# Kernel tuning notes

Measured on AMD Instinct MI355X. Metric: run time of the kernel, lower is better.

The kernel has to match this reference:

```python
import jax, jax.numpy as jnp
import numpy as np

D_MODEL = 1024
N_HEAD = 16
D_K = D_MODEL // N_HEAD
B, S = 2, 2048


def setup_inputs() -> dict:
    key = jax.random.key(0)
    ks = jax.random.split(key, 12)
    sc = 1.0 / np.sqrt(D_MODEL)
    return {
        "q": jax.random.normal(ks[0], (B, S, D_MODEL), jnp.float32),
        "k": jax.random.normal(ks[1], (B, S, D_MODEL), jnp.float32),
        "v": jax.random.normal(ks[2], (B, S, D_MODEL), jnp.float32),
        "mask": jax.random.randint(ks[3], (B, S, S), 0, 2, jnp.int32),
        # learned params (torch Linear convention: y = x @ W + b with W pre-transposed)
        "wq": jax.random.normal(ks[4], (D_MODEL, D_MODEL), jnp.float32) * sc,
        "bq": jax.random.normal(ks[5], (D_MODEL,), jnp.float32) * sc,
        "wk": jax.random.normal(ks[6], (D_MODEL, D_MODEL), jnp.float32) * sc,  # no bias
        "wv": jax.random.normal(ks[7], (D_MODEL, D_MODEL), jnp.float32) * sc,
        "bv": jax.random.normal(ks[8], (D_MODEL,), jnp.float32) * sc,
        "wf": jax.random.normal(ks[9], (D_MODEL, D_MODEL), jnp.float32) * sc,
        "bf": jax.random.normal(ks[10], (D_MODEL,), jnp.float32) * sc,
    }


def reference(q, k, v, mask, wq, bq, wk, wv, bv, wf, bf):
    bs = q.shape[0]
    temperature = jnp.asarray(D_K ** 0.5, q.dtype)
    # projections -> [b, h, s, d_k]
    qh = (q @ wq + bq).reshape(bs, -1, N_HEAD, D_K).transpose(0, 2, 1, 3)
    kh = (k @ wk).reshape(bs, -1, N_HEAD, D_K).transpose(0, 2, 1, 3)
    vh = (v @ wv + bv).reshape(bs, -1, N_HEAD, D_K).transpose(0, 2, 1, 3)
    # scores [b, h, sq, sk]
    attn = jnp.einsum("bhqd,bhkd->bhqk", qh, kh) / temperature
    m0 = (mask[:, None, :, :] == 0)  # mask==0 -> masked out, broadcast over heads
    attn = jnp.where(m0, -jnp.inf, attn)
    attn = jax.nn.softmax(attn, axis=-1)
    attn = jnp.where(m0, 0.0, attn)
    out = jnp.einsum("bhqk,bhkd->bhqd", attn, vh)
    out = out.transpose(0, 2, 1, 3).reshape(bs, -1, D_MODEL)
    return out @ wf + bf  # dropout is identity in eval mode
```

## Files before the change

kernel.cpp:

```cpp
#include <hip/hip_runtime.h>

#define D_MODEL 1024
#define NHEAD   16
#define DK      64
#define BATCH   2
#define SEQ     2048

typedef __attribute__((ext_vector_type(8))) short bf16x8;
typedef __attribute__((ext_vector_type(4))) short bf16x4;
typedef __attribute__((ext_vector_type(4))) float f32x4;
typedef __attribute__((ext_vector_type(2))) int i32x2;

#define QSCALE 0.18033688011f

__device__ __forceinline__ unsigned short f2b(float x) {
  unsigned u = __builtin_bit_cast(unsigned, x);
  u = (u + 0x7fffu + ((u >> 16) & 1u)) >> 16;
  return (unsigned short)u;
}
__device__ __forceinline__ unsigned short f2b_rhu(float x) {
  return (unsigned short)((__builtin_bit_cast(unsigned, x) + 0x8000u) >> 16);
}
__device__ __forceinline__ int pk2(float a, float b) {
  unsigned ua = __builtin_bit_cast(unsigned, a) + 0x8000u;
  unsigned ub = __builtin_bit_cast(unsigned, b) + 0x8000u;
  return (int)__builtin_amdgcn_perm(ub, ua, 0x07060302u);
}
__device__ __forceinline__ int pk2u(unsigned ua, unsigned ub) {
  return (int)__builtin_amdgcn_perm(ub + 0x8000u, ua + 0x8000u, 0x07060302u);
}

typedef const __attribute__((address_space(1))) void* gas_p;
typedef __attribute__((address_space(3))) void* las_p;
__device__ __forceinline__ void gll16(const void* g, void* l) {
  __builtin_amdgcn_global_load_lds((gas_p)g, (las_p)l, 16, 0, 0);
}

__device__ __forceinline__ f32x4 mfma16(bf16x4 a, bf16x4 b, f32x4 c) {
#if __has_builtin(__builtin_amdgcn_mfma_f32_16x16x16bf16_1k)
  return __builtin_amdgcn_mfma_f32_16x16x16bf16_1k(a, b, c, 0, 0, 0);
#else
  f32x4 d;
  asm("v_mfma_f32_16x16x16_bf16 %0, %1, %2, %3" : "=v"(d) : "v"(a), "v"(b), "v"(c));
  return d;
#endif
}

__global__ __launch_bounds__(256) void prep_kernel(
    const float* __restrict__ q, const float* __restrict__ k, const float* __restrict__ v,
    unsigned short* __restrict__ qb, unsigned short* __restrict__ kb,
    unsigned short* __restrict__ vb,
    const float* __restrict__ wq, const float* __restrict__ wk,
    const float* __restrict__ wv, const float* __restrict__ wf,
    unsigned short* __restrict__ wqt, unsigned short* __restrict__ wkt,
    unsigned short* __restrict__ wvt, unsigned short* __restrict__ wft,
    const int* __restrict__ mask, unsigned long long* __restrict__ mbits) {
  int bid = blockIdx.x, t = threadIdx.x;
  if (bid < 6144) {
    int by = bid >> 11, bx = bid & 2047;
    const float* src = by == 0 ? q : (by == 1 ? k : v);
    unsigned short* dst = by == 0 ? qb : (by == 1 ? kb : vb);
    size_t i = ((size_t)bx * 256 + t) * 8;
    float4 x0 = *(const float4*)&src[i];
    float4 x1 = *(const float4*)&src[i + 4];
    int4 w;
    w.x = pk2(x0.x, x0.y); w.y = pk2(x0.z, x0.w);
    w.z = pk2(x1.x, x1.y); w.w = pk2(x1.z, x1.w);
    *(int4*)&dst[i] = w;
  } else if (bid < 7168) {
    __shared__ float tile[64][65];
    int idx = bid - 6144;
    int bz = idx >> 8, by = (idx >> 4) & 15, bx = idx & 15;
    const float* w; unsigned short* wt;
    switch (bz) {
      case 0: w = wq; wt = wqt; break;
      case 1: w = wk; wt = wkt; break;
      case 2: w = wv; wt = wvt; break;
      default: w = wf; wt = wft; break;
    }
    int r0 = by * 64, c0 = bx * 64;
    for (int i = 0; i < 16; ++i) {
      int idx2 = t + i * 256; int r = idx2 >> 6, c = idx2 & 63;
      tile[r][c] = w[(size_t)(r0 + r) * D_MODEL + c0 + c];
    }
    __syncthreads();
    for (int i = 0; i < 16; ++i) {
      int idx2 = t + i * 256; int r = idx2 >> 6, c = idx2 & 63;
      wt[(size_t)(c0 + r) * D_MODEL + r0 + c] = f2b(tile[c][r]);
    }
  } else {
    int idx = bid - 7168;
    int lane = t & 63, wave = t >> 6;
    size_t base = ((size_t)idx * 4 + wave) * 256;
    unsigned long long b0 = __ballot(mask[base + lane] != 0);
    unsigned long long b1 = __ballot(mask[base + 64 + lane] != 0);
    unsigned long long b2 = __ballot(mask[base + 128 + lane] != 0);
    unsigned long long b3 = __ballot(mask[base + 192 + lane] != 0);
    if (lane == 0) {
      unsigned long long* p = &mbits[(size_t)idx * 16 + wave * 4];
      p[0] = b0; p[1] = b1; p[2] = b2; p[3] = b3;
    }
  }
}

__global__ __launch_bounds__(256) void gemm_qkv_kernel(
    const unsigned short* __restrict__ qb, const unsigned short* __restrict__ kb,
    const unsigned short* __restrict__ vb,
    const unsigned short* __restrict__ wqt, const unsigned short* __restrict__ wkt,
    const unsigned short* __restrict__ wvt,
    const float* __restrict__ bq, const float* __restrict__ bv,
    unsigned short* __restrict__ qh, unsigned short* __restrict__ kh,
    unsigned short* __restrict__ vt) {
  __shared__ unsigned short SB[16640];
  int bid = blockIdx.x;
  int xcd = bid & 7, slot = bid >> 3;
  int mi = slot & 3, zn = slot >> 2;
  int z = zn >> 3;
  int n0 = (zn & 7) * 128;
  int m0 = (mi * 8 + xcd) * 128;
  const unsigned short* A; const unsigned short* Bt;
  switch (z) {
    case 0:  A = qb; Bt = wqt; break;
    case 1:  A = kb; Bt = wkt; break;
    default: A = vb; Bt = wvt; break;
  }
  int t = threadIdx.x, lane = t & 63, wave = t >> 6;
  int l16 = lane & 15, quad = lane >> 4;
  int wm = (wave & 1) * 64, wn = (wave >> 1) * 64;
  f32x4 zero = {0.f, 0.f, 0.f, 0.f};
  f32x4 acc[4][4];
  for (int mt = 0; mt < 4; ++mt) for (int nt = 0; nt < 4; ++nt) acc[mt][nt] = zero;

  int drow = lane >> 2, dcol = (lane & 3) * 8;
  const unsigned short* asrc = A  + (size_t)(m0 + wave * 32 + drow) * D_MODEL + dcol;
  const unsigned short* bsrc = Bt + (size_t)(n0 + wave * 32 + drow) * D_MODEL + dcol;
  int dst = wave * 1024 + lane * 8;

#pragma unroll
  for (int g = 0; g < 2; ++g) {
    gll16(asrc + (size_t)(g * 16) * D_MODEL, &SB[dst + g * 512]);
    gll16(bsrc + (size_t)(g * 16) * D_MODEL, &SB[4096 + dst + g * 512]);
  }
  for (int it = 0; it < 32; ++it) {
    __syncthreads();
    if (it + 1 < 32) {
      int nb = ((it + 1) & 1) * 8192, kn = (it + 1) * 32;
#pragma unroll
      for (int g = 0; g < 2; ++g) {
        gll16(asrc + (size_t)(g * 16) * D_MODEL + kn, &SB[nb + dst + g * 512]);
        gll16(bsrc + (size_t)(g * 16) * D_MODEL + kn, &SB[nb + 4096 + dst + g * 512]);
      }
    }
    int cb = (it & 1) * 8192;
    bf16x8 a[4], b[4];
    for (int mt = 0; mt < 4; ++mt)
      a[mt] = *(const bf16x8*)&SB[cb + (wm + mt * 16 + l16) * 32 + quad * 8];
    for (int nt = 0; nt < 4; ++nt)
      b[nt] = *(const bf16x8*)&SB[cb + 4096 + (wn + nt * 16 + l16) * 32 + quad * 8];
    for (int mt = 0; mt < 4; ++mt)
      for (int nt = 0; nt < 4; ++nt)
        acc[mt][nt] = __builtin_amdgcn_mfma_f32_16x16x32_bf16(a[mt], b[nt], acc[mt][nt], 0, 0, 0);
  }

  if (z == 2) {
    __syncthreads();
#pragma unroll
    for (int nt = 0; nt < 4; ++nt) {
      int col = wn + nt * 16 + l16;
      float bb = bv[n0 + col];
      for (int mt = 0; mt < 4; ++mt)
        for (int r = 0; r < 4; ++r)
          SB[col * 130 + wm + mt * 16 + quad * 4 + r] = f2b_rhu(acc[mt][nt][r] + bb);
    }
    __syncthreads();
    int c = t >> 1, hf = t & 1;
    int colg = n0 + c, hh = colg >> 6, dd = colg & 63;
    int b_ = m0 >> 11, sbase = m0 & (SEQ - 1);
    unsigned short* dstp = vt + (((size_t)(b_ * NHEAD + hh)) * DK + dd) * SEQ + sbase + hf * 64;
#pragma unroll
    for (int j = 0; j < 8; ++j)
      *(int4*)(dstp + j * 8) = *(const int4*)&SB[c * 130 + hf * 64 + j * 8];
  } else {
    __syncthreads();
#pragma unroll
    for (int nt = 0; nt < 4; ++nt) {
      int lcol = wn + nt * 16 + l16;
      float bb = (z == 0) ? bq[n0 + lcol] : 0.f;
      for (int mt = 0; mt < 4; ++mt)
        for (int r = 0; r < 4; ++r) {
          float val = acc[mt][nt][r] + bb;
          if (z == 0) val *= QSCALE;
          SB[(wm + mt * 16 + quad * 4 + r) * 130 + lcol] = f2b_rhu(val);
        }
    }
    __syncthreads();
    unsigned short* outp = (z == 0) ? qh : kh;
    int b_ = m0 >> 11, sbase = m0 & (SEQ - 1);
    int h0 = n0 >> 6, c = t & 7;
#pragma unroll
    for (int pass = 0; pass < 8; ++pass) {
      int rp = pass * 32 + (t >> 3);
      int srow = rp >> 1, part = rp & 1;
      unsigned short* dstp = outp +
          (((size_t)(b_ * NHEAD + h0 + part)) * SEQ + sbase + srow) * DK + c * 8;
      *(int4*)dstp = *(const int4*)&SB[srow * 130 + part * 64 + c * 8];
    }
  }
}

__global__ __launch_bounds__(256) void gemm_out_kernel(
    const unsigned short* __restrict__ A, const unsigned short* __restrict__ Bt,
    const float* __restrict__ bias, float* __restrict__ out) {
  __shared__ unsigned short As[8192], Bs[8192];
  int bid = blockIdx.x;
  int xcd = bid & 7, slot = bid >> 3;
  int mi = slot & 7, n0 = (slot >> 3) * 64;
  int m0 = (mi * 8 + xcd) * 64;
  int t = threadIdx.x, lane = t & 63, wave = t >> 6;
  int l16 = lane & 15, quad = lane >> 4;
  int wm = (wave & 1) * 32, wn = (wave >> 1) * 32;
  f32x4 zero = {0.f, 0.f, 0.f, 0.f};
  f32x4 acc[2][2];
  for (int mt = 0; mt < 2; ++mt) for (int nt = 0; nt < 2; ++nt) acc[mt][nt] = zero;

  int drow = lane >> 2, dcol = (lane & 3) * 8;
  const unsigned short* asrc = A  + (size_t)(m0 + wave * 16 + drow) * D_MODEL + dcol;
  const unsigned short* bsrc = Bt + (size_t)(n0 + wave * 16 + drow) * D_MODEL + dcol;
  int dst = wave * 512 + lane * 8;

#pragma unroll
  for (int hf = 0; hf < 2; ++hf) {
    gll16(asrc + hf * 32, &As[dst + hf * 2048]);
    gll16(bsrc + hf * 32, &Bs[dst + hf * 2048]);
  }
  for (int it = 0; it < 16; ++it) {
    __syncthreads();
    if (it + 1 < 16) {
      int nb = ((it + 1) & 1) * 4096, kn = (it + 1) * 64;
#pragma unroll
      for (int hf = 0; hf < 2; ++hf) {
        gll16(asrc + kn + hf * 32, &As[nb + dst + hf * 2048]);
        gll16(bsrc + kn + hf * 32, &Bs[nb + dst + hf * 2048]);
      }
    }
    int cb = (it & 1) * 4096;
#pragma unroll
    for (int half = 0; half < 2; ++half) {
      bf16x8 a[2], b[2];
      for (int mt = 0; mt < 2; ++mt)
        a[mt] = *(const bf16x8*)&As[cb + half * 2048 + (wm + mt * 16 + l16) * 32 + quad * 8];
      for (int nt = 0; nt < 2; ++nt)
        b[nt] = *(const bf16x8*)&Bs[cb + half * 2048 + (wn + nt * 16 + l16) * 32 + quad * 8];
      for (int mt = 0; mt < 2; ++mt)
        for (int nt = 0; nt < 2; ++nt)
          acc[mt][nt] = __builtin_amdgcn_mfma_f32_16x16x32_bf16(a[mt], b[nt], acc[mt][nt], 0, 0, 0);
    }
  }
  for (int nt = 0; nt < 2; ++nt) {
    int col = n0 + wn + nt * 16 + l16;
    float bb = bias[col];
    for (int mt = 0; mt < 2; ++mt)
      for (int r = 0; r < 4; ++r) {
        int row = m0 + wm + mt * 16 + quad * 4 + r;
        out[(size_t)row * D_MODEL + col] = acc[mt][nt][r] + bb;
      }
  }
}

__global__ __launch_bounds__(128, 2) void attn_kernel(
    const unsigned short* __restrict__ qh, const unsigned short* __restrict__ kh,
    const unsigned short* __restrict__ vt, const unsigned long long* __restrict__ mbits,
    unsigned short* __restrict__ attb) {
  __shared__ unsigned short Ks[8192];
  __shared__ unsigned short Vs[8192];
  int bid = blockIdx.x;
  int xcd = bid & 7, slot = bid >> 3;
  int bh_ = 4 * xcd + (slot >> 5);
  int qt = slot & 31;
  int b = bh_ >> 4, h = bh_ & 15;
  int t = threadIdx.x, lane = t & 63, wave = t >> 6;
  int l16 = lane & 15, quad = lane >> 4;
  size_t bh = (size_t)b * NHEAD + h;

  const unsigned short* Kg = kh + bh * SEQ * DK;
  const unsigned short* Vg = vt + bh * DK * SEQ;
  const unsigned long long* mrow = mbits + (size_t)b * SEQ * (SEQ / 64);
  int qrowb = qt * 64 + wave * 32;

  bf16x8 qf[2][2];
#pragma unroll
  for (int qm = 0; qm < 2; ++qm) {
    const unsigned short* Qg = qh + (bh * SEQ + (size_t)(qrowb + qm * 16 + l16)) * DK;
    qf[qm][0] = *(const bf16x8*)&Qg[quad * 8];
    qf[qm][1] = *(const bf16x8*)&Qg[32 + quad * 8];
  }

  int srow8 = t >> 3;
  int schk = ((t & 7) ^ (srow8 & 7)) * 8;
  const unsigned short* ksrc = Kg + (size_t)srow8 * DK + schk;
  const unsigned short* vsrc = Vg + (size_t)srow8 * SEQ + schk;
  int sdst = t * 8;

  int x7 = l16 & 7;
  int ka0 = l16 * 64 + ((quad ^ x7) * 8);
  int ka1 = l16 * 64 + (((4 + quad) ^ x7) * 8);
  int va[4];
#pragma unroll
  for (int nt = 0; nt < 4; ++nt)
    va[nt] = l16 * 64 + (((nt * 2 + (quad >> 1)) ^ x7) * 8) + (quad & 1) * 4;

  size_t mi0 = (size_t)(qrowb + l16) * (SEQ / 64);
  size_t mi1 = (size_t)(qrowb + 16 + l16) * (SEQ / 64);

  bf16x4 ones4;
#pragma unroll
  for (int i = 0; i < 4; ++i) ones4[i] = (short)0x3F80;

  f32x4 zero = {0.f, 0.f, 0.f, 0.f};
  f32x4 accO[2][4], accRS[2];
#pragma unroll
  for (int qm = 0; qm < 2; ++qm) {
    accRS[qm] = zero;
    for (int dt = 0; dt < 4; ++dt) accO[qm][dt] = zero;
  }

#pragma unroll
  for (int g = 0; g < 4; ++g) {
    gll16(ksrc + (size_t)(g * 16) * DK, &Ks[g * 1024 + sdst]);
    gll16(vsrc + (size_t)(g * 16) * SEQ, &Vs[g * 1024 + sdst]);
  }

  for (int tk = 0; tk < SEQ / 64; ++tk) {
    __syncthreads();
    if (tk + 1 < SEQ / 64) {
      int nb = ((tk + 1) & 1) * 4096;
      const unsigned short* kn = ksrc + (size_t)((tk + 1) * 64) * DK;
      const unsigned short* vn = vsrc + (tk + 1) * 64;
#pragma unroll
      for (int g = 0; g < 4; ++g) {
        gll16(kn + (size_t)(g * 16) * DK, &Ks[nb + g * 1024 + sdst]);
        gll16(vn + (size_t)(g * 16) * SEQ, &Vs[nb + g * 1024 + sdst]);
      }
    }
    unsigned long long mq0 = mrow[mi0 + tk];
    unsigned long long mq1 = mrow[mi1 + tk];

    int cb = (tk & 1) * 4096;

    f32x4 accS[2][4];
#pragma unroll
    for (int qm = 0; qm < 2; ++qm)
      for (int nt = 0; nt < 4; ++nt) accS[qm][nt] = zero;
#pragma unroll
    for (int step = 0; step < 2; ++step) {
      int ka = step ? ka1 : ka0;
#pragma unroll
      for (int nt = 0; nt < 4; ++nt) {
        bf16x8 kf = *(const bf16x8*)&Ks[cb + ka + nt * 1024];
        accS[0][nt] = __builtin_amdgcn_mfma_f32_16x16x32_bf16(kf, qf[0][step], accS[0][nt], 0, 0, 0);
        accS[1][nt] = __builtin_amdgcn_mfma_f32_16x16x32_bf16(kf, qf[1][step], accS[1][nt], 0, 0, 0);
      }
    }

    bf16x4 ap[2][4];
#pragma unroll
    for (int qm = 0; qm < 2; ++qm) {
      unsigned long long mq = (qm ? mq1 : mq0) >> (quad * 4);
      unsigned mlo = (unsigned)mq, mhi = (unsigned)(mq >> 32);
#pragma unroll
      for (int nt = 0; nt < 4; ++nt) {
        unsigned w = (nt < 2) ? mlo : mhi;
        unsigned pu[4];
#pragma unroll
        for (int r = 0; r < 4; ++r) {
          float pv = __builtin_amdgcn_exp2f(accS[qm][nt][r]);
          int msk = ((int)(w << (31 - ((nt & 1) * 16 + r)))) >> 31;
          pu[r] = __builtin_bit_cast(unsigned, pv) & (unsigned)msk;
        }
        i32x2 wv;
        wv[0] = pk2u(pu[0], pu[1]);
        wv[1] = pk2u(pu[2], pu[3]);
        ap[qm][nt] = __builtin_bit_cast(bf16x4, wv);
      }
#pragma unroll
      for (int nt = 0; nt < 4; ++nt)
        accRS[qm] = mfma16(ap[qm][nt], ones4, accRS[qm]);
    }

#pragma unroll
    for (int nt = 0; nt < 4; ++nt) {
      int vb_ = cb + va[nt];
#pragma unroll
      for (int dt = 0; dt < 4; ++dt) {
        bf16x4 vf = *(const bf16x4*)&Vs[vb_ + dt * 1024];
        accO[0][dt] = mfma16(ap[0][nt], vf, accO[0][dt]);
        accO[1][dt] = mfma16(ap[1][nt], vf, accO[1][dt]);
      }
    }
  }

#pragma unroll
  for (int qm = 0; qm < 2; ++qm)
    for (int r = 0; r < 4; ++r) {
      float sden = accRS[qm][r];
      float inv = sden > 0.f ? 1.f / sden : 0.f;
      int row = qrowb + qm * 16 + quad * 4 + r;
      size_t ob = ((size_t)b * SEQ + row) * D_MODEL + (size_t)h * DK;
      for (int dt = 0; dt < 4; ++dt)
        attb[ob + dt * 16 + l16] = f2b_rhu(accO[qm][dt][r] * inv);
    }
}

extern "C" void kernel_launch(void* const* d_in, const int* in_sizes, int n_in,
                              void* d_out, int out_size, void* d_ws, size_t ws_size,
                              hipStream_t stream) {
  (void)in_sizes; (void)n_in; (void)out_size; (void)ws_size;
  const float* q    = (const float*)d_in[0];
  const float* k    = (const float*)d_in[1];
  const float* v    = (const float*)d_in[2];
  const int*   mask = (const int*)d_in[3];
  const float* wq   = (const float*)d_in[4];
  const float* bq   = (const float*)d_in[5];
  const float* wk   = (const float*)d_in[6];
  const float* wv   = (const float*)d_in[7];
  const float* bv   = (const float*)d_in[8];
  const float* wf   = (const float*)d_in[9];
  const float* bf   = (const float*)d_in[10];

  char* ws = (char*)d_ws;
  unsigned short* wft  = (unsigned short*)(ws + 0);
  unsigned short* wqt  = (unsigned short*)(ws + 2097152);
  unsigned short* wkt  = (unsigned short*)(ws + 4194304);
  unsigned short* wvt  = (unsigned short*)(ws + 6291456);
  unsigned short* attb = (unsigned short*)(ws + 2097152);
  unsigned short* qhp  = (unsigned short*)(ws + 10485760);
  unsigned short* khp  = (unsigned short*)(ws + 18874368);
  unsigned short* vtp  = (unsigned short*)(ws + 27262976);
  unsigned long long* mbits = (unsigned long long*)(ws + 35651584);
  unsigned short* vb   = (unsigned short*)(ws + 36700160);
  unsigned short* qb   = (unsigned short*)d_out;
  unsigned short* kb   = (unsigned short*)d_out + 4194304;

  hipLaunchKernelGGL(prep_kernel, dim3(15360), dim3(256), 0, stream,
                     q, k, v, qb, kb, vb,
                     wq, wk, wv, wf, wqt, wkt, wvt, wft, mask, mbits);
  hipLaunchKernelGGL(gemm_qkv_kernel, dim3(768), dim3(256), 0, stream,
                     qb, kb, vb, wqt, wkt, wvt, bq, bv, qhp, khp, vtp);
  hipLaunchKernelGGL(attn_kernel, dim3(1024), dim3(128), 0, stream,
                     qhp, khp, vtp, mbits, attb);
  hipLaunchKernelGGL(gemm_out_kernel, dim3(1024), dim3(256), 0, stream,
                     attb, wft, bf, (float*)d_out);
}
```

Baseline: 268.0 us.

## Widen attention tiles to 128 queries and 128 keys per block with 4 waves

```diff
diff --git a/kernel.cpp b/kernel.cpp
--- a/kernel.cpp
+++ b/kernel.cpp
@@ -267,16 +267,16 @@
   }
 }
 
-__global__ __launch_bounds__(128, 2) void attn_kernel(
+__global__ __launch_bounds__(256, 2) void attn_kernel(
     const unsigned short* __restrict__ qh, const unsigned short* __restrict__ kh,
     const unsigned short* __restrict__ vt, const unsigned long long* __restrict__ mbits,
     unsigned short* __restrict__ attb) {
-  __shared__ unsigned short Ks[8192];
-  __shared__ unsigned short Vs[8192];
+  __shared__ unsigned short Ks[16384];
+  __shared__ unsigned short Vs[16384];
   int bid = blockIdx.x;
   int xcd = bid & 7, slot = bid >> 3;
-  int bh_ = 4 * xcd + (slot >> 5);
-  int qt = slot & 31;
+  int bh_ = 4 * xcd + (slot >> 4);
+  int qt = slot & 15;
   int b = bh_ >> 4, h = bh_ & 15;
   int t = threadIdx.x, lane = t & 63, wave = t >> 6;
   int l16 = lane & 15, quad = lane >> 4;
@@ -285,7 +285,7 @@
   const unsigned short* Kg = kh + bh * SEQ * DK;
   const unsigned short* Vg = vt + bh * DK * SEQ;
   const unsigned long long* mrow = mbits + (size_t)b * SEQ * (SEQ / 64);
-  int qrowb = qt * 64 + wave * 32;
+  int qrowb = qt * 128 + wave * 32;
 
   bf16x8 qf[2][2];
 #pragma unroll
@@ -295,19 +295,24 @@
     qf[qm][1] = *(const bf16x8*)&Qg[32 + quad * 8];
   }
 
-  int srow8 = t >> 3;
-  int schk = ((t & 7) ^ (srow8 & 7)) * 8;
-  const unsigned short* ksrc = Kg + (size_t)srow8 * DK + schk;
-  const unsigned short* vsrc = Vg + (size_t)srow8 * SEQ + schk;
+  int ksrow = t >> 3;
+  int kschk = ((t & 7) ^ (ksrow & 7)) * 8;
+  const unsigned short* ksrc = Kg + (size_t)ksrow * DK + kschk;
+  int vsrow = t >> 4;
+  int vschk = ((t & 15) ^ (vsrow & 15)) * 8;
+  const unsigned short* vsrc = Vg + (size_t)vsrow * SEQ + vschk;
   int sdst = t * 8;
 
   int x7 = l16 & 7;
   int ka0 = l16 * 64 + ((quad ^ x7) * 8);
   int ka1 = l16 * 64 + (((4 + quad) ^ x7) * 8);
-  int va[4];
-#pragma unroll
-  for (int nt = 0; nt < 4; ++nt)
-    va[nt] = l16 * 64 + (((nt * 2 + (quad >> 1)) ^ x7) * 8) + (quad & 1) * 4;
+  int va[2][4];
+#pragma unroll
+  for (int sub = 0; sub < 2; ++sub)
+#pragma unroll
+    for (int nt = 0; nt < 4; ++nt)
+      va[sub][nt] = l16 * 128 + (((sub * 8 + nt * 2 + (quad >> 1)) ^ l16) * 8)
+                    + (quad & 1) * 4;
 
   size_t mi0 = (size_t)(qrowb + l16) * (SEQ / 64);
   size_t mi1 = (size_t)(qrowb + 16 + l16) * (SEQ / 64);
@@ -326,75 +331,82 @@
 
 #pragma unroll
   for (int g = 0; g < 4; ++g) {
-    gll16(ksrc + (size_t)(g * 16) * DK, &Ks[g * 1024 + sdst]);
-    gll16(vsrc + (size_t)(g * 16) * SEQ, &Vs[g * 1024 + sdst]);
-  }
-
-  for (int tk = 0; tk < SEQ / 64; ++tk) {
-    __syncthreads();
-    if (tk + 1 < SEQ / 64) {
-      int nb = ((tk + 1) & 1) * 4096;
-      const unsigned short* kn = ksrc + (size_t)((tk + 1) * 64) * DK;
-      const unsigned short* vn = vsrc + (tk + 1) * 64;
+    gll16(ksrc + (size_t)(g * 32) * DK, &Ks[g * 2048 + sdst]);
+    gll16(vsrc + (size_t)(g * 16) * SEQ, &Vs[g * 2048 + sdst]);
+  }
+
+  for (int tk = 0; tk < SEQ / 128; ++tk) {
+    __syncthreads();
+    if (tk + 1 < SEQ / 128) {
+      int nb = ((tk + 1) & 1) * 8192;
+      const unsigned short* kn = ksrc + (size_t)(tk + 1) * 128 * DK;
+      const unsigned short* vn = vsrc + (tk + 1) * 128;
 #pragma unroll
       for (int g = 0; g < 4; ++g) {
-        gll16(kn + (size_t)(g * 16) * DK, &Ks[nb + g * 1024 + sdst]);
-        gll16(vn + (size_t)(g * 16) * SEQ, &Vs[nb + g * 1024 + sdst]);
-      }
-    }
-    unsigned long long mq0 = mrow[mi0 + tk];
-    unsigned long long mq1 = mrow[mi1 + tk];
-
-    int cb = (tk & 1) * 4096;
-
-    f32x4 accS[2][4];
-#pragma unroll
-    for (int qm = 0; qm < 2; ++qm)
-      for (int nt = 0; nt < 4; ++nt) accS[qm][nt] = zero;
-#pragma unroll
-    for (int step = 0; step < 2; ++step) {
-      int ka = step ? ka1 : ka0;
+        gll16(kn + (size_t)(g * 32) * DK, &Ks[nb + g * 2048 + sdst]);
+        gll16(vn + (size_t)(g * 16) * SEQ, &Vs[nb + g * 2048 + sdst]);
+      }
+    }
+    unsigned long long mA0 = mrow[mi0 + 2 * tk];
+    unsigned long long mA1 = mrow[mi0 + 2 * tk + 1];
+    unsigned long long mB0 = mrow[mi1 + 2 * tk];
+    unsigned long long mB1 = mrow[mi1 + 2 * tk + 1];
+
+    int cb = (tk & 1) * 8192;
+#pragma unroll
+    for (int sub = 0; sub < 2; ++sub) {
+      int kb_ = cb + sub * 4096;
+      f32x4 accS[2][4];
+#pragma unroll
+      for (int qm = 0; qm < 2; ++qm)
+        for (int nt = 0; nt < 4; ++nt) accS[qm][nt] = zero;
+#pragma unroll
+      for (int step = 0; step < 2; ++step) {
+        int ka = step ? ka1 : ka0;
+#pragma unroll
+        for (int nt = 0; nt < 4; ++nt) {
+          bf16x8 kf = *(const bf16x8*)&Ks[kb_ + ka + nt * 1024];
+          accS[0][nt] = __builtin_amdgcn_mfma_f32_16x16x32_bf16(kf, qf[0][step], accS[0][nt], 0, 0, 0);
+          accS[1][nt] = __builtin_amdgcn_mfma_f32_16x16x32_bf16(kf, qf[1][step], accS[1][nt], 0, 0, 0);
+        }
+      }
+
+      unsigned long long ms0 = sub ? mA1 : mA0;
+      unsigned long long ms1 = sub ? mB1 : mB0;
+      bf16x4 ap[2][4];
+#pragma unroll
+      for (int qm = 0; qm < 2; ++qm) {
+        unsigned long long mq = (qm ? ms1 : ms0) >> (quad * 4);
+        unsigned mlo = (unsigned)mq, mhi = (unsigned)(mq >> 32);
+#pragma unroll
+        for (int nt = 0; nt < 4; ++nt) {
+          unsigned w = (nt < 2) ? mlo : mhi;
+          unsigned pu[4];
+#pragma unroll
+          for (int r = 0; r < 4; ++r) {
+            float pv = __builtin_amdgcn_exp2f(accS[qm][nt][r]);
+            int msk = ((int)(w << (31 - ((nt & 1) * 16 + r)))) >> 31;
+            pu[r] = __builtin_bit_cast(unsigned, pv) & (unsigned)msk;
+          }
+          i32x2 wv;
+          wv[0] = pk2u(pu[0], pu[1]);
+          wv[1] = pk2u(pu[2], pu[3]);
+          ap[qm][nt] = __builtin_bit_cast(bf16x4, wv);
+        }
+#pragma unroll
+        for (int nt = 0; nt < 4; ++nt)
+          accRS[qm] = mfma16(ap[qm][nt], ones4, accRS[qm]);
+      }
+
 #pragma unroll
       for (int nt = 0; nt < 4; ++nt) {
-        bf16x8 kf = *(const bf16x8*)&Ks[cb + ka + nt * 1024];
-        accS[0][nt] = __builtin_amdgcn_mfma_f32_16x16x32_bf16(kf, qf[0][step], accS[0][nt], 0, 0, 0);
-        accS[1][nt] = __builtin_amdgcn_mfma_f32_16x16x32_bf16(kf, qf[1][step], accS[1][nt], 0, 0, 0);
-      }
-    }
-
-    bf16x4 ap[2][4];
-#pragma unroll
-    for (int qm = 0; qm < 2; ++qm) {
-      unsigned long long mq = (qm ? mq1 : mq0) >> (quad * 4);
-      unsigned mlo = (unsigned)mq, mhi = (unsigned)(mq >> 32);
-#pragma unroll
-      for (int nt = 0; nt < 4; ++nt) {
-        unsigned w = (nt < 2) ? mlo : mhi;
-        unsigned pu[4];
-#pragma unroll
-        for (int r = 0; r < 4; ++r) {
-          float pv = __builtin_amdgcn_exp2f(accS[qm][nt][r]);
-          int msk = ((int)(w << (31 - ((nt & 1) * 16 + r)))) >> 31;
-          pu[r] = __builtin_bit_cast(unsigned, pv) & (unsigned)msk;
+        int vb_ = cb + va[sub][nt];
+#pragma unroll
+        for (int dt = 0; dt < 4; ++dt) {
+          bf16x4 vf = *(const bf16x4*)&Vs[vb_ + dt * 2048];
+          accO[0][dt] = mfma16(ap[0][nt], vf, accO[0][dt]);
+          accO[1][dt] = mfma16(ap[1][nt], vf, accO[1][dt]);
         }
-        i32x2 wv;
-        wv[0] = pk2u(pu[0], pu[1]);
-        wv[1] = pk2u(pu[2], pu[3]);
-        ap[qm][nt] = __builtin_bit_cast(bf16x4, wv);
-      }
-#pragma unroll
-      for (int nt = 0; nt < 4; ++nt)
-        accRS[qm] = mfma16(ap[qm][nt], ones4, accRS[qm]);
-    }
-
-#pragma unroll
-    for (int nt = 0; nt < 4; ++nt) {
-      int vb_ = cb + va[nt];
-#pragma unroll
-      for (int dt = 0; dt < 4; ++dt) {
-        bf16x4 vf = *(const bf16x4*)&Vs[vb_ + dt * 1024];
-        accO[0][dt] = mfma16(ap[0][nt], vf, accO[0][dt]);
-        accO[1][dt] = mfma16(ap[1][nt], vf, accO[1][dt]);
       }
     }
   }
@@ -446,7 +458,7 @@
                      wq, wk, wv, wf, wqt, wkt, wvt, wft, mask, mbits);
   hipLaunchKernelGGL(gemm_qkv_kernel, dim3(768), dim3(256), 0, stream,
                      qb, kb, vb, wqt, wkt, wvt, bq, bv, qhp, khp, vtp);
-  hipLaunchKernelGGL(attn_kernel, dim3(1024), dim3(128), 0, stream,
+  hipLaunchKernelGGL(attn_kernel, dim3(512), dim3(256), 0, stream,
                      qhp, khp, vtp, mbits, attb);
   hipLaunchKernelGGL(gemm_out_kernel, dim3(1024), dim3(256), 0, stream,
                      attb, wft, bf, (float*)d_out);
```

After: 261.7 us. -2.4%, faster.
